# Performance work log

Measured on AMD Instinct MI355X. Metric: run time of the kernel, lower is better.

## Reference

```python
import jax, jax.numpy as jnp
import numpy as np

N_ATOM = 10000
N_EDGE = 40000
D = 64          # fingerprint_dim
BOND_DIM = 10
EPS_BN = 1e-6
EPS_SM = 1e-8


def _bn(x, g, b, m, v):
    # BatchNorm1d in eval mode with running stats
    return (x - m) * jax.lax.rsqrt(v + EPS_BN) * g + b


def setup_inputs() -> dict:
    key = jax.random.key(0)
    ks = jax.random.split(key, 16)
    s = 0.05
    inp = {
        "atom": jax.random.normal(ks[0], (N_ATOM, D), jnp.float32),
        "bond_index": jax.random.randint(ks[1], (N_EDGE, 2), 0, N_ATOM, jnp.int64),
        "bond": jax.random.normal(ks[2], (N_EDGE, BOND_DIM), jnp.float32),
        # encoder: Linear(bond_dim, D*D) + BN(D*D)
        "enc_W": jax.random.normal(ks[3], (D * D, BOND_DIM), jnp.float32) * s,
        "enc_b": jnp.zeros((D * D,), jnp.float32),
        "bn1_g": jnp.ones((D * D,), jnp.float32),
        "bn1_b": jnp.zeros((D * D,), jnp.float32),
        "bn1_m": jnp.zeros((D * D,), jnp.float32),
        "bn1_v": jnp.ones((D * D,), jnp.float32),
        # align: Linear(2D, 1)
        "align_W": jax.random.normal(ks[4], (1, 2 * D), jnp.float32) * s,
        "align_b": jnp.zeros((1,), jnp.float32),
        # attend: Linear(D, D) + BN(D)
        "att_W": jax.random.normal(ks[5], (D, D), jnp.float32) * s,
        "att_b": jnp.zeros((D,), jnp.float32),
        "bn2_g": jnp.ones((D,), jnp.float32),
        "bn2_b": jnp.zeros((D,), jnp.float32),
        "bn2_m": jnp.zeros((D,), jnp.float32),
        "bn2_v": jnp.ones((D,), jnp.float32),
        # GRUCell(D, D)
        "gru_Wih": jax.random.normal(ks[6], (3 * D, D), jnp.float32) * s,
        "gru_Whh": jax.random.normal(ks[7], (3 * D, D), jnp.float32) * s,
        "gru_bih": jnp.zeros((3 * D,), jnp.float32),
        "gru_bhh": jnp.zeros((3 * D,), jnp.float32),
    }
    return inp


def reference(atom, bond_index, bond, enc_W, enc_b, bn1_g, bn1_b, bn1_m, bn1_v,
              align_W, align_b, att_W, att_b, bn2_g, bn2_b, bn2_m, bn2_v,
              gru_Wih, gru_Whh, gru_bih, gru_bhh):
    num_atom, atom_dim = atom.shape
    tgt = bond_index[:, 0]  # segment index (bond_index.t()[0])
    nbr = bond_index[:, 1]

    # encoder: Linear + BN + ReLU, then view as per-edge [D, D] matrices
    enc = jax.nn.relu(_bn(bond @ enc_W.T + enc_b, bn1_g, bn1_b, bn1_m, bn1_v))
    enc = enc.reshape(-1, atom_dim, atom_dim)            # [E, D, D]

    neighbor = jnp.einsum('ed,edf->ef', atom[nbr], enc)  # per-edge bmm [E, D]
    target_atom = atom[tgt]

    feat = jnp.concatenate([target_atom, neighbor], axis=-1)       # [E, 2D]
    align_score = jax.nn.leaky_relu(feat @ align_W.T + align_b)    # [E, 1]

    atend = _bn(neighbor @ att_W.T + att_b, bn2_g, bn2_b, bn2_m, bn2_v)  # [E, D]

    # segment softmax over edges grouped by target atom
    seg_max = jax.ops.segment_max(align_score, tgt, num_segments=num_atom)
    ex = jnp.exp(align_score - seg_max[tgt])
    denom = jax.ops.segment_sum(ex, tgt, num_segments=num_atom)[tgt] + EPS_SM
    w = ex / denom                                                   # [E, 1]

    context = jax.ops.segment_sum(w * atend, tgt, num_segments=num_atom)  # [N, D]
    context = jax.nn.elu(context)

    # GRUCell(context, atom)
    gi = context @ gru_Wih.T + gru_bih
    gh = atom @ gru_Whh.T + gru_bhh
    i_r, i_z, i_n = jnp.split(gi, 3, axis=-1)
    h_r, h_z, h_n = jnp.split(gh, 3, axis=-1)
    r = jax.nn.sigmoid(i_r + h_r)
    z = jax.nn.sigmoid(i_z + h_z)
    n = jnp.tanh(i_n + r * h_n)
    update = (1.0 - z) * n + z * atom
    return update
```

## Files before the change

kernel.cpp:

```cpp
#include <hip/hip_runtime.h>

#define N_ATOM 10000
#define N_EDGE 40000
#define DD 64
#define BOND_DIM 10
#define EPS_BN 1e-6f
#define EPS_SM 1e-8f
#define GA 8

typedef __attribute__((ext_vector_type(8))) short short8;
typedef __attribute__((ext_vector_type(4))) float float4v;
typedef unsigned int u32;

constexpr size_t OFF_WFRAG   = 0;
constexpr size_t OFF_ATTFRAG = 65536;
constexpr size_t OFF_ATTB    = 67584;
constexpr size_t OFF_WIHT    = 67648;
constexpr size_t OFF_WHHT    = 79936;
constexpr size_t OFF_DENOM   = 92224;
constexpr size_t OFF_CTX     = 102224;

__device__ __forceinline__ unsigned short f2bf(float x) {
    u32 u = __float_as_uint(x);
    u32 r = u + 0x7FFFu + ((u >> 16) & 1u);
    return (unsigned short)(r >> 16);
}

__global__ void fold_kernel(const float* enc_W, const float* enc_b,
                            const float* g1, const float* b1,
                            const float* m1, const float* v1,
                            const float* att_W, const float* att_b,
                            const float* g2, const float* b2v,
                            const float* m2, const float* v2,
                            const float* Wih, const float* Whh,
                            float* ws) {
    u32* wsu = (u32*)ws;
    size_t i = (size_t)blockIdx.x * 256 + threadIdx.x;
    if (i < 16384) {
        int ch = i >> 6, l = i & 63, q = l >> 4;
        int c = (ch << 4) + (l & 15);
        float s = g1[c] * rsqrtf(v1[c] + EPS_BN);
        float bias = enc_b[c] * s + b1[c] - m1[c] * s;
        unsigned short h[8];
#pragma unroll
        for (int j = 0; j < 8; j++) {
            int k = 8 * q + j;
            float v = (k < BOND_DIM) ? enc_W[c * BOND_DIM + k] * s
                                     : ((k == BOND_DIM) ? bias : 0.f);
            h[j] = f2bf(v);
        }
#pragma unroll
        for (int m = 0; m < 4; m++)
            wsu[OFF_WFRAG + i * 4 + m] = (u32)h[2 * m] | ((u32)h[2 * m + 1] << 16);
    } else if (i < 16896) {
        int idx = i - 16384;
        int l = idx & 63, fckh = idx >> 6;
        int fc = fckh >> 1, kh = fckh & 1, q = l >> 4;
        int n = (fc << 4) + (l & 15);
        float s = g2[n] * rsqrtf(v2[n] + EPS_BN);
        unsigned short h[8];
#pragma unroll
        for (int j = 0; j < 8; j++) {
            int k = 32 * kh + 8 * q + j;
            h[j] = f2bf(att_W[n * DD + k] * s);
        }
#pragma unroll
        for (int m = 0; m < 4; m++)
            wsu[OFF_ATTFRAG + (size_t)idx * 4 + m] = (u32)h[2 * m] | ((u32)h[2 * m + 1] << 16);
    } else if (i < 16960) {
        int f = i - 16896;
        float s = g2[f] * rsqrtf(v2[f] + EPS_BN);
        ws[OFF_ATTB + f] = att_b[f] * s + b2v[f] - m2[f] * s;
    } else if (i < 29248) {
        int j = i - 16960;
        int d = j / 192, t = j % 192;
        ws[OFF_WIHT + j] = Wih[t * DD + d];
    } else if (i < 41536) {
        int j = i - 29248;
        int d = j / 192, t = j % 192;
        ws[OFF_WHHT + j] = Whh[t * DD + d];
    } else {
        size_t z = i - 41536;
        if (z < (size_t)N_ATOM + (size_t)N_ATOM * DD) ws[OFF_DENOM + z] = 0.f;
    }
}

__global__ __launch_bounds__(256) void edge_kernel(
    const float* atom, const int* bidx, const float* bond,
    const float* alignW, const float* alignb,
    const float* ws, float* denom, float* ctx) {
    __shared__ float s_anbr[64][65];
    __shared__ float s_nb[64][65];
    __shared__ float s_bond[64][BOND_DIM];
    __shared__ float s_ex[64];
    __shared__ int   s_tgt[64];

    const int t = threadIdx.x;
    const int lane = t & 63;
    const int wave = t >> 6;
    const int q = lane >> 4;
    const int r16 = lane & 15;
    const int we0 = wave * 16;
    const int ew = blockIdx.x * 64 + we0;

    for (int idx = lane; idx < 16 * BOND_DIM; idx += 64)
        s_bond[we0 + idx / BOND_DIM][idx % BOND_DIM] = bond[(size_t)ew * BOND_DIM + idx];
#pragma unroll 4
    for (int j = 0; j < 16; j++) {
        int nbr = bidx[2 * (ew + j) + 1];
        s_anbr[we0 + j][lane] = atom[(size_t)nbr * DD + lane];
    }

    short8 afrag;
#pragma unroll
    for (int j = 0; j < 8; j++) {
        int k = 8 * q + j;
        unsigned short h = 0;
        if (k < BOND_DIM) h = f2bf(s_bond[we0 + r16][k]);
        else if (k == BOND_DIM) h = 0x3F80u;
        afrag[j] = (short)h;
    }

    const short8* wfrag = (const short8*)((const u32*)ws + OFF_WFRAG);
    const float4v zero4 = {0.f, 0.f, 0.f, 0.f};
    float4v nacc[4] = {zero4, zero4, zero4, zero4};

#pragma unroll 2
    for (int d = 0; d < DD; d++) {
        float av0 = s_anbr[we0 + 4 * q + 0][d];
        float av1 = s_anbr[we0 + 4 * q + 1][d];
        float av2 = s_anbr[we0 + 4 * q + 2][d];
        float av3 = s_anbr[we0 + 4 * q + 3][d];
#pragma unroll
        for (int fc = 0; fc < 4; fc++) {
            short8 bfr = wfrag[(size_t)(d * 4 + fc) * 64 + lane];
            float4v e4 = __builtin_amdgcn_mfma_f32_16x16x32_bf16(afrag, bfr, zero4, 0, 0, 0);
            nacc[fc][0] = fmaf(av0, fmaxf(e4[0], 0.f), nacc[fc][0]);
            nacc[fc][1] = fmaf(av1, fmaxf(e4[1], 0.f), nacc[fc][1]);
            nacc[fc][2] = fmaf(av2, fmaxf(e4[2], 0.f), nacc[fc][2]);
            nacc[fc][3] = fmaf(av3, fmaxf(e4[3], 0.f), nacc[fc][3]);
        }
    }

#pragma unroll
    for (int fc = 0; fc < 4; fc++)
#pragma unroll
        for (int r = 0; r < 4; r++)
            s_nb[we0 + 4 * q + r][fc * 16 + r16] = nacc[fc][r];

    short8 na[2];
#pragma unroll
    for (int kh = 0; kh < 2; kh++) {
#pragma unroll
        for (int j = 0; j < 8; j++)
            na[kh][j] = (short)f2bf(s_nb[we0 + r16][32 * kh + 8 * q + j]);
    }
    const short8* battfrag = (const short8*)((const u32*)ws + OFF_ATTFRAG);
    float4v att[4];
#pragma unroll
    for (int fc = 0; fc < 4; fc++) {
        att[fc] = __builtin_amdgcn_mfma_f32_16x16x32_bf16(na[0], battfrag[(fc * 2 + 0) * 64 + lane], zero4, 0, 0, 0);
        att[fc] = __builtin_amdgcn_mfma_f32_16x16x32_bf16(na[1], battfrag[(fc * 2 + 1) * 64 + lane], att[fc], 0, 0, 0);
        float ab = ws[OFF_ATTB + fc * 16 + r16];
#pragma unroll
        for (int r = 0; r < 4; r++) att[fc][r] += ab;
    }

    const float aw1 = alignW[lane];
    const float aw2 = alignW[64 + lane];
    const float alb = alignb[0];
#pragma unroll 4
    for (int e = 0; e < 16; e++) {
        int tgt = bidx[2 * (ew + e)];
        float v = atom[(size_t)tgt * DD + lane] * aw1 + s_nb[we0 + e][lane] * aw2;
#pragma unroll
        for (int off = 32; off > 0; off >>= 1) v += __shfl_xor(v, off);
        float sc = v + alb;
        sc = sc > 0.f ? sc : 0.01f * sc;
        float ex = expf(sc);
        if (lane == 0) {
            s_ex[we0 + e] = ex;
            s_tgt[we0 + e] = tgt;
            atomicAdd(&denom[tgt], ex);
        }
    }

#pragma unroll
    for (int r = 0; r < 4; r++) {
        float exr = s_ex[we0 + 4 * q + r];
        int tg = s_tgt[we0 + 4 * q + r];
#pragma unroll
        for (int fc = 0; fc < 4; fc++)
            atomicAdd(&ctx[(size_t)tg * DD + fc * 16 + r16], exr * att[fc][r]);
    }
}

__global__ __launch_bounds__(192) void gru_kernel(
    const float* atom, const float* ws, const float* denom, const float* ctx,
    const float* bih, const float* bhh, float* out) {
    __shared__ float sctx[GA][DD];
    __shared__ float satom[GA][DD];
    __shared__ float sgi[GA][192];
    __shared__ float sgh[GA][192];
    const int a0 = blockIdx.x * GA;
    const int t = threadIdx.x;

    for (int idx = t; idx < GA * DD; idx += 192) {
        int a = idx >> 6, f = idx & 63;
        float c = ctx[(size_t)(a0 + a) * DD + f] / (denom[a0 + a] + EPS_SM);
        sctx[a][f] = c > 0.f ? c : expm1f(c);
        satom[a][f] = atom[(size_t)(a0 + a) * DD + f];
    }
    __syncthreads();

    const float* wiht = ws + OFF_WIHT;
    const float* whht = ws + OFF_WHHT;
    float gi[GA], gh[GA];
    const float bi = bih[t], bh = bhh[t];
#pragma unroll
    for (int a = 0; a < GA; a++) { gi[a] = bi; gh[a] = bh; }
#pragma unroll 4
    for (int d = 0; d < DD; d++) {
        float wi = wiht[d * 192 + t];
        float wh = whht[d * 192 + t];
#pragma unroll
        for (int a = 0; a < GA; a++) {
            gi[a] = fmaf(wi, sctx[a][d], gi[a]);
            gh[a] = fmaf(wh, satom[a][d], gh[a]);
        }
    }
#pragma unroll
    for (int a = 0; a < GA; a++) { sgi[a][t] = gi[a]; sgh[a][t] = gh[a]; }
    __syncthreads();

    for (int idx = t; idx < GA * DD; idx += 192) {
        int a = idx >> 6, f = idx & 63;
        float r = 1.f / (1.f + expf(-(sgi[a][f] + sgh[a][f])));
        float z = 1.f / (1.f + expf(-(sgi[a][64 + f] + sgh[a][64 + f])));
        float n = tanhf(sgi[a][128 + f] + r * sgh[a][128 + f]);
        out[(size_t)(a0 + a) * DD + f] = (1.f - z) * n + z * satom[a][f];
    }
}

extern "C" void kernel_launch(void* const* d_in, const int* in_sizes, int n_in,
                              void* d_out, int out_size, void* d_ws, size_t ws_size,
                              hipStream_t stream) {
    const float* atom   = (const float*)d_in[0];
    const int*   bidx   = (const int*)d_in[1];
    const float* bond   = (const float*)d_in[2];
    const float* enc_W  = (const float*)d_in[3];
    const float* enc_b  = (const float*)d_in[4];
    const float* bn1_g  = (const float*)d_in[5];
    const float* bn1_b  = (const float*)d_in[6];
    const float* bn1_m  = (const float*)d_in[7];
    const float* bn1_v  = (const float*)d_in[8];
    const float* alignW = (const float*)d_in[9];
    const float* alignb = (const float*)d_in[10];
    const float* att_W  = (const float*)d_in[11];
    const float* att_b  = (const float*)d_in[12];
    const float* bn2_g  = (const float*)d_in[13];
    const float* bn2_b  = (const float*)d_in[14];
    const float* bn2_m  = (const float*)d_in[15];
    const float* bn2_v  = (const float*)d_in[16];
    const float* gWih   = (const float*)d_in[17];
    const float* gWhh   = (const float*)d_in[18];
    const float* gbih   = (const float*)d_in[19];
    const float* gbhh   = (const float*)d_in[20];

    float* ws  = (float*)d_ws;
    float* out = (float*)d_out;

    fold_kernel<<<2702, 256, 0, stream>>>(enc_W, enc_b, bn1_g, bn1_b, bn1_m, bn1_v,
                                          att_W, att_b, bn2_g, bn2_b, bn2_m, bn2_v,
                                          gWih, gWhh, ws);

    edge_kernel<<<N_EDGE / 64, 256, 0, stream>>>(
        atom, bidx, bond, alignW, alignb, ws,
        ws + OFF_DENOM, ws + OFF_CTX);

    gru_kernel<<<N_ATOM / GA, 192, 0, stream>>>(atom, ws, ws + OFF_DENOM, ws + OFF_CTX,
                                                gbih, gbhh, out);
}
```

Measured before the change: 167.8 us.

## Split edge kernel reduction dimension across wave pairs with prefetched weight fragments

```diff
diff --git a/kernel.cpp b/kernel.cpp
--- a/kernel.cpp
+++ b/kernel.cpp
@@ -89,109 +89,133 @@
     const float* atom, const int* bidx, const float* bond,
     const float* alignW, const float* alignb,
     const float* ws, float* denom, float* ctx) {
-    __shared__ float s_anbr[64][65];
-    __shared__ float s_nb[64][65];
-    __shared__ float s_bond[64][BOND_DIM];
-    __shared__ float s_ex[64];
-    __shared__ int   s_tgt[64];
+    __shared__ float s_bond[32][BOND_DIM];
+    __shared__ float s_anbr[32][65];
+    __shared__ float s_nbp[2][32][65];
+    __shared__ float s_ex[32];
+    __shared__ int   s_tgt[32];
 
     const int t = threadIdx.x;
     const int lane = t & 63;
     const int wave = t >> 6;
+    const int g = wave >> 1;
+    const int h = wave & 1;
     const int q = lane >> 4;
     const int r16 = lane & 15;
-    const int we0 = wave * 16;
-    const int ew = blockIdx.x * 64 + we0;
-
-    for (int idx = lane; idx < 16 * BOND_DIM; idx += 64)
-        s_bond[we0 + idx / BOND_DIM][idx % BOND_DIM] = bond[(size_t)ew * BOND_DIM + idx];
-#pragma unroll 4
-    for (int j = 0; j < 16; j++) {
-        int nbr = bidx[2 * (ew + j) + 1];
-        s_anbr[we0 + j][lane] = atom[(size_t)nbr * DD + lane];
-    }
+    const int g16 = g * 16;
+    const int e0 = blockIdx.x * 32;
+
+    for (int idx = t; idx < 32 * BOND_DIM; idx += 256)
+        s_bond[idx / BOND_DIM][idx % BOND_DIM] = bond[(size_t)e0 * BOND_DIM + idx];
+    if (t < 32) s_tgt[t] = bidx[2 * (e0 + t)];
+    for (int e = wave; e < 32; e += 4) {
+        int nbr = bidx[2 * (e0 + e) + 1];
+        s_anbr[e][lane] = atom[(size_t)nbr * DD + lane];
+    }
+    __syncthreads();
 
     short8 afrag;
 #pragma unroll
     for (int j = 0; j < 8; j++) {
         int k = 8 * q + j;
-        unsigned short h = 0;
-        if (k < BOND_DIM) h = f2bf(s_bond[we0 + r16][k]);
-        else if (k == BOND_DIM) h = 0x3F80u;
-        afrag[j] = (short)h;
+        unsigned short hh = 0;
+        if (k < BOND_DIM) hh = f2bf(s_bond[g16 + r16][k]);
+        else if (k == BOND_DIM) hh = 0x3F80u;
+        afrag[j] = (short)hh;
     }
 
     const short8* wfrag = (const short8*)((const u32*)ws + OFF_WFRAG);
     const float4v zero4 = {0.f, 0.f, 0.f, 0.f};
     float4v nacc[4] = {zero4, zero4, zero4, zero4};
-
-#pragma unroll 2
-    for (int d = 0; d < DD; d++) {
-        float av0 = s_anbr[we0 + 4 * q + 0][d];
-        float av1 = s_anbr[we0 + 4 * q + 1][d];
-        float av2 = s_anbr[we0 + 4 * q + 2][d];
-        float av3 = s_anbr[we0 + 4 * q + 3][d];
+    const int d0 = 32 * h;
+
+    auto compute = [&](const short8 cur[4], int d) {
+        float av0 = s_anbr[g16 + 4 * q + 0][d];
+        float av1 = s_anbr[g16 + 4 * q + 1][d];
+        float av2 = s_anbr[g16 + 4 * q + 2][d];
+        float av3 = s_anbr[g16 + 4 * q + 3][d];
 #pragma unroll
         for (int fc = 0; fc < 4; fc++) {
-            short8 bfr = wfrag[(size_t)(d * 4 + fc) * 64 + lane];
-            float4v e4 = __builtin_amdgcn_mfma_f32_16x16x32_bf16(afrag, bfr, zero4, 0, 0, 0);
+            float4v e4 = __builtin_amdgcn_mfma_f32_16x16x32_bf16(afrag, cur[fc], zero4, 0, 0, 0);
             nacc[fc][0] = fmaf(av0, fmaxf(e4[0], 0.f), nacc[fc][0]);
             nacc[fc][1] = fmaf(av1, fmaxf(e4[1], 0.f), nacc[fc][1]);
             nacc[fc][2] = fmaf(av2, fmaxf(e4[2], 0.f), nacc[fc][2]);
             nacc[fc][3] = fmaf(av3, fmaxf(e4[3], 0.f), nacc[fc][3]);
         }
-    }
+    };
+
+    short8 cur[4], nxt[4];
+#pragma unroll
+    for (int fc = 0; fc < 4; fc++) cur[fc] = wfrag[(size_t)(d0 * 4 + fc) * 64 + lane];
+#pragma unroll 2
+    for (int it = 0; it < 31; it++) {
+        int d = d0 + it;
+#pragma unroll
+        for (int fc = 0; fc < 4; fc++) nxt[fc] = wfrag[(size_t)((d + 1) * 4 + fc) * 64 + lane];
+        compute(cur, d);
+#pragma unroll
+        for (int fc = 0; fc < 4; fc++) cur[fc] = nxt[fc];
+    }
+    compute(cur, d0 + 31);
 
 #pragma unroll
     for (int fc = 0; fc < 4; fc++)
 #pragma unroll
         for (int r = 0; r < 4; r++)
-            s_nb[we0 + 4 * q + r][fc * 16 + r16] = nacc[fc][r];
-
-    short8 na[2];
-#pragma unroll
-    for (int kh = 0; kh < 2; kh++) {
-#pragma unroll
-        for (int j = 0; j < 8; j++)
-            na[kh][j] = (short)f2bf(s_nb[we0 + r16][32 * kh + 8 * q + j]);
-    }
-    const short8* battfrag = (const short8*)((const u32*)ws + OFF_ATTFRAG);
+            s_nbp[h][g16 + 4 * q + r][fc * 16 + r16] = nacc[fc][r];
+    __syncthreads();
+
     float4v att[4];
-#pragma unroll
-    for (int fc = 0; fc < 4; fc++) {
-        att[fc] = __builtin_amdgcn_mfma_f32_16x16x32_bf16(na[0], battfrag[(fc * 2 + 0) * 64 + lane], zero4, 0, 0, 0);
-        att[fc] = __builtin_amdgcn_mfma_f32_16x16x32_bf16(na[1], battfrag[(fc * 2 + 1) * 64 + lane], att[fc], 0, 0, 0);
-        float ab = ws[OFF_ATTB + fc * 16 + r16];
-#pragma unroll
-        for (int r = 0; r < 4; r++) att[fc][r] += ab;
-    }
-
-    const float aw1 = alignW[lane];
-    const float aw2 = alignW[64 + lane];
-    const float alb = alignb[0];
+    if (h == 0) {
+        short8 na[2];
+#pragma unroll
+        for (int kh = 0; kh < 2; kh++)
+#pragma unroll
+            for (int j = 0; j < 8; j++) {
+                int k = 32 * kh + 8 * q + j;
+                na[kh][j] = (short)f2bf(s_nbp[0][g16 + r16][k] + s_nbp[1][g16 + r16][k]);
+            }
+        const short8* battfrag = (const short8*)((const u32*)ws + OFF_ATTFRAG);
+#pragma unroll
+        for (int fc = 0; fc < 4; fc++) {
+            att[fc] = __builtin_amdgcn_mfma_f32_16x16x32_bf16(na[0], battfrag[(fc * 2 + 0) * 64 + lane], zero4, 0, 0, 0);
+            att[fc] = __builtin_amdgcn_mfma_f32_16x16x32_bf16(na[1], battfrag[(fc * 2 + 1) * 64 + lane], att[fc], 0, 0, 0);
+            float ab = ws[OFF_ATTB + fc * 16 + r16];
+#pragma unroll
+            for (int r = 0; r < 4; r++) att[fc][r] += ab;
+        }
+    } else {
+        const float aw1 = alignW[lane];
+        const float aw2 = alignW[64 + lane];
+        const float alb = alignb[0];
 #pragma unroll 4
-    for (int e = 0; e < 16; e++) {
-        int tgt = bidx[2 * (ew + e)];
-        float v = atom[(size_t)tgt * DD + lane] * aw1 + s_nb[we0 + e][lane] * aw2;
-#pragma unroll
-        for (int off = 32; off > 0; off >>= 1) v += __shfl_xor(v, off);
-        float sc = v + alb;
-        sc = sc > 0.f ? sc : 0.01f * sc;
-        float ex = expf(sc);
-        if (lane == 0) {
-            s_ex[we0 + e] = ex;
-            s_tgt[we0 + e] = tgt;
-            atomicAdd(&denom[tgt], ex);
-        }
-    }
-
-#pragma unroll
-    for (int r = 0; r < 4; r++) {
-        float exr = s_ex[we0 + 4 * q + r];
-        int tg = s_tgt[we0 + 4 * q + r];
-#pragma unroll
-        for (int fc = 0; fc < 4; fc++)
-            atomicAdd(&ctx[(size_t)tg * DD + fc * 16 + r16], exr * att[fc][r]);
+        for (int e = 0; e < 16; e++) {
+            int le = g16 + e;
+            int tgt = s_tgt[le];
+            float nbv = s_nbp[0][le][lane] + s_nbp[1][le][lane];
+            float v = atom[(size_t)tgt * DD + lane] * aw1 + nbv * aw2;
+#pragma unroll
+            for (int off = 32; off > 0; off >>= 1) v += __shfl_xor(v, off);
+            float sc = v + alb;
+            sc = sc > 0.f ? sc : 0.01f * sc;
+            float ex = expf(sc);
+            if (lane == 0) {
+                s_ex[le] = ex;
+                atomicAdd(&denom[tgt], ex);
+            }
+        }
+    }
+    __syncthreads();
+
+    if (h == 0) {
+#pragma unroll
+        for (int r = 0; r < 4; r++) {
+            float exr = s_ex[g16 + 4 * q + r];
+            int tg = s_tgt[g16 + 4 * q + r];
+#pragma unroll
+            for (int fc = 0; fc < 4; fc++)
+                atomicAdd(&ctx[(size_t)tg * DD + fc * 16 + r16], exr * att[fc][r]);
+        }
     }
 }
 
@@ -274,7 +298,7 @@
                                           att_W, att_b, bn2_g, bn2_b, bn2_m, bn2_v,
                                           gWih, gWhh, ws);
 
-    edge_kernel<<<N_EDGE / 64, 256, 0, stream>>>(
+    edge_kernel<<<N_EDGE / 32, 256, 0, stream>>>(
         atom, bidx, bond, alignW, alignb, ws,
         ws + OFF_DENOM, ws + OFF_CTX);
 
```

Measured after the change: 163.3 us. 2.7% less time.
